# Kernel tuning notes

Hardware: AMD Instinct MI355X
Metric: run time of the kernel (lower is better)

## Reference

```python
import jax, jax.numpy as jnp
import numpy as np

COST_CLASS, COST_MASK, COST_DICE = 2.0, 5.0, 5.0
NUM_POINTS = 12544

def setup_inputs() -> dict:
    key = jax.random.key(0)
    k1, k2, k3, k4, k5 = jax.random.split(key, 5)
    bs, Q, K = 4, 100, 134
    H = W = 256
    M = 80
    P = H * W
    pred_logits = jax.random.normal(k1, (bs, Q, K), dtype=jnp.float32)
    pred_masks = jax.random.normal(k2, (bs, Q, H, W), dtype=jnp.float32)
    tgt_labels = jax.random.randint(k3, (M,), 0, K - 1, dtype=jnp.int32)
    # binary target masks, stored as float (matches .float() in torch code)
    tgt_masks = (jax.random.uniform(k4, (M, H, W)) > 0.5).astype(jnp.float32)
    # random subset of points without replacement (torch.randperm[:num_points])
    point_idx = jax.random.permutation(k5, P)[:NUM_POINTS].astype(jnp.int32)
    return {"pred_logits": pred_logits, "pred_masks": pred_masks,
            "tgt_labels": tgt_labels, "tgt_masks": tgt_masks,
            "point_idx": point_idx}

def reference(pred_logits, pred_masks, tgt_labels, tgt_masks, point_idx):
    bs, Q, K = pred_logits.shape
    N = bs * Q
    M = tgt_masks.shape[0]
    Pn = point_idx.shape[0]

    # class cost: -p[n, tgt_id[m]]
    out_prob = jax.nn.softmax(pred_logits.reshape(N, K), axis=-1)
    tgt_ids = jnp.clip(tgt_labels.astype(jnp.int32), 0, K - 1)
    cost_class = -out_prob[:, tgt_ids]                      # (N, M)

    # sampled mask logits / targets
    x = pred_masks.reshape(N, -1)[:, point_idx]             # (N, Pn) logits
    y = tgt_masks.reshape(M, -1)[:, point_idx]              # (M, Pn) binary float

    # BCE-with-logits cost, separable form:
    # mean_p[softplus(x) - x*y] = mean_p softplus(x) - (x @ y^T)/Pn
    sp_mean = jnp.mean(jax.nn.softplus(x), axis=-1)         # (N,)
    xy = jnp.einsum('np,mp->nm', x, y)                      # (N, M)
    cost_mask = sp_mean[:, None] - xy / Pn

    # dice cost
    s = jax.nn.sigmoid(x)                                   # (N, Pn)
    numer = 2.0 * jnp.einsum('np,mp->nm', s, y)             # (N, M)
    denom = jnp.sum(s, axis=-1)[:, None] + jnp.sum(y, axis=-1)[None, :]
    cost_dice = 1.0 - (numer + 1.0) / (denom + 1.0)

    C = COST_CLASS * cost_class + COST_MASK * cost_mask + COST_DICE * cost_dice
    return C.reshape(bs, Q, M)
```

## Files before the change

### kernel.cpp

```cpp
#include <hip/hip_runtime.h>
#include <math.h>

#define N_ROWS 400
#define M_ROWS 80
#define K_CLS  134
#define PN     12544
#define PFULL  65536
#define NSUB   25
#define TSTEPS 392
#define KSPLIT 196
#define TPB    2
#define KCG    49

#define GY_BLOCKS 245

typedef __attribute__((ext_vector_type(4))) float  f32x4;
typedef __attribute__((ext_vector_type(8))) __bf16 bf16x8;

__device__ __forceinline__ float wave_reduce_sum(float v) {
#pragma unroll
    for (int off = 32; off > 0; off >>= 1) v += __shfl_down(v, off, 64);
    return v;
}

__global__ __launch_bounds__(1024) void sort_softmax_kernel(
        const int* __restrict__ point_idx, int* __restrict__ sel,
        const float* __restrict__ pred_logits,
        float* __restrict__ rowmax, float* __restrict__ rowsum) {
    int tid = threadIdx.x;
    if (blockIdx.x == 0) {
        __shared__ unsigned int bits[PFULL / 32];
        __shared__ int wtot[16], wbase[16];
        bits[tid] = 0u; bits[tid + 1024] = 0u;
        __syncthreads();
        for (int i = tid; i < PN; i += 1024) {
            int p = point_idx[i];
            atomicOr(&bits[p >> 5], 1u << (p & 31));
        }
        __syncthreads();
        unsigned int w0 = bits[tid * 2], w1 = bits[tid * 2 + 1];
        int cnt = __popc(w0) + __popc(w1);
        int lane = tid & 63, wid = tid >> 6;
        int v = cnt;
#pragma unroll
        for (int off = 1; off < 64; off <<= 1) {
            int u = __shfl_up(v, off, 64);
            if (lane >= off) v += u;
        }
        if (lane == 63) wtot[wid] = v;
        __syncthreads();
        if (tid == 0) {
            int run = 0;
#pragma unroll
            for (int i = 0; i < 16; ++i) { wbase[i] = run; run += wtot[i]; }
        }
        __syncthreads();
        int base = wbase[wid] + (v - cnt);
        int p0 = tid * 64;
        while (w0) { int b = __builtin_ctz(w0); w0 &= w0 - 1; sel[base++] = p0 + b; }
        p0 += 32;
        while (w1) { int b = __builtin_ctz(w1); w1 &= w1 - 1; sel[base++] = p0 + b; }
    } else {
        int wave = tid >> 6, lane = tid & 63;
        int n = (blockIdx.x - 1) * 16 + wave;
        const float* row = pred_logits + n * K_CLS;
        float mx = -1e30f;
        for (int k = lane; k < K_CLS; k += 64) mx = fmaxf(mx, row[k]);
#pragma unroll
        for (int off = 32; off > 0; off >>= 1) mx = fmaxf(mx, __shfl_down(mx, off, 64));
        mx = __shfl(mx, 0, 64);
        float se = 0.f;
        for (int k = lane; k < K_CLS; k += 64) se += expf(row[k] - mx);
        se = wave_reduce_sum(se);
        if (lane == 0) { rowmax[n] = mx; rowsum[n] = se; }
    }
}

__global__ __launch_bounds__(512) void gather_y_kernel(
        const float* __restrict__ tgt_masks, const int* __restrict__ sel,
        __bf16* __restrict__ Yb, float* __restrict__ ypart) {
    __shared__ float smem[128];
    int b = blockIdx.x;
    int j = b / 49, tch = b % 49;
    int wave = threadIdx.x >> 6, lane = threadIdx.x & 63;
    int colL = lane & 15, quad = lane >> 4;
    int m = 16 * j + colL;
    int t = tch * 8 + wave;
    int k0 = t * 32 + quad * 8;
    const float* yrow = tgt_masks + (size_t)m * PFULL;
    int idx[8];
    *(int4*)(idx)     = *(const int4*)(sel + k0);
    *(int4*)(idx + 4) = *(const int4*)(sel + k0 + 4);
    bf16x8 v; float acc = 0.f;
#pragma unroll
    for (int jj = 0; jj < 8; ++jj) {
        float y = yrow[idx[jj]];
        v[jj] = (__bf16)y;
        acc += y;
    }
    ((bf16x8*)Yb)[(size_t)(t * 5 + j) * 64 + lane] = v;
    acc += __shfl_down(acc, 32, 64);
    acc += __shfl_down(acc, 16, 64);
    if (quad == 0) smem[wave * 16 + colL] = acc;
    __syncthreads();
    if (threadIdx.x < 16) {
        float s = 0.f;
#pragma unroll
        for (int wv = 0; wv < 8; ++wv) s += smem[wv * 16 + threadIdx.x];
        ypart[tch * M_ROWS + 16 * j + threadIdx.x] = s;
    }
}

__global__ __launch_bounds__(256) void gemm_fused_kernel(
        const float* __restrict__ pred_masks, const int* __restrict__ sel,
        const __bf16* __restrict__ Yb,
        float* __restrict__ xypart, float* __restrict__ sypart,
        float* __restrict__ rowS, float* __restrict__ rowSP) {
    __shared__ float red[4][40][64];
    __shared__ float rowred[4][2][16];
    int wave = threadIdx.x >> 6, lane = threadIdx.x & 63;
    int nsub = blockIdx.x / KCG, kcg = blockIdx.x % KCG;
    int kc = kcg * 4 + wave;
    int n0 = nsub * 16;
    int colL = lane & 15, quad = lane >> 4;
    int tbase = kc * TPB;

    const float* row = pred_masks + (size_t)(n0 + colL) * PFULL;
    const bf16x8* Yfrag = (const bf16x8*)Yb;

    f32x4 accX[5], accS[5];
    f32x4 zero = {0.f, 0.f, 0.f, 0.f};
#pragma unroll
    for (int j = 0; j < 5; ++j) { accX[j] = zero; accS[j] = zero; }
    float sumS = 0.f, sumSP = 0.f;

    float xs[TPB][8];
    bf16x8 Bbuf[TPB][5];
#pragma unroll
    for (int i = 0; i < TPB; ++i) {
        int t = tbase + i;
        int k0 = t * 32 + quad * 8;
        int idx[8];
        *(int4*)(idx)     = *(const int4*)(sel + k0);
        *(int4*)(idx + 4) = *(const int4*)(sel + k0 + 4);
#pragma unroll
        for (int jj = 0; jj < 8; ++jj) xs[i][jj] = row[idx[jj]];
        const bf16x8* q = Yfrag + (size_t)(t * 5) * 64 + lane;
#pragma unroll
        for (int j = 0; j < 5; ++j) Bbuf[i][j] = q[(size_t)j * 64];
    }
#pragma unroll
    for (int i = 0; i < TPB; ++i) {
        bf16x8 aX, aS;
#pragma unroll
        for (int jj = 0; jj < 8; ++jj) {
            float x  = xs[i][jj];
            float ax = fabsf(x);
            float e  = __expf(-ax);
            float inv = __builtin_amdgcn_rcpf(1.f + e);
            float sig = (x >= 0.f) ? inv : e * inv;
            float sp  = fmaxf(x, 0.f) + __logf(1.f + e);
            aX[jj] = (__bf16)x; aS[jj] = (__bf16)sig;
            sumS += sig; sumSP += sp;
        }
#pragma unroll
        for (int j = 0; j < 5; ++j) {
            accX[j] = __builtin_amdgcn_mfma_f32_16x16x32_bf16(aX, Bbuf[i][j], accX[j], 0, 0, 0);
            accS[j] = __builtin_amdgcn_mfma_f32_16x16x32_bf16(aS, Bbuf[i][j], accS[j], 0, 0, 0);
        }
    }

#pragma unroll
    for (int j = 0; j < 5; ++j)
#pragma unroll
        for (int r = 0; r < 4; ++r) {
            red[wave][j * 4 + r][lane]      = accX[j][r];
            red[wave][20 + j * 4 + r][lane] = accS[j][r];
        }
    sumS  += __shfl_down(sumS, 32, 64);
    sumS  += __shfl_down(sumS, 16, 64);
    sumSP += __shfl_down(sumSP, 32, 64);
    sumSP += __shfl_down(sumSP, 16, 64);
    if (lane < 16) { rowred[wave][0][lane] = sumS; rowred[wave][1][lane] = sumSP; }
    __syncthreads();
#pragma unroll
    for (int v0 = 0; v0 < 10; ++v0) {
        int v = wave * 10 + v0;
        float s = red[0][v][lane] + red[1][v][lane] + red[2][v][lane] + red[3][v][lane];
        int vv = (v < 20) ? v : v - 20;
        int j = vv >> 2, r = vv & 3;
        int n = n0 + quad * 4 + r, m = 16 * j + colL;
        float* dst = (v < 20) ? xypart : sypart;
        dst[(size_t)kcg * (N_ROWS * M_ROWS) + n * M_ROWS + m] = s;
    }
    if (threadIdx.x < 16) {
        rowS[kcg * N_ROWS + n0 + threadIdx.x] =
            rowred[0][0][threadIdx.x] + rowred[1][0][threadIdx.x] +
            rowred[2][0][threadIdx.x] + rowred[3][0][threadIdx.x];
    } else if (threadIdx.x < 32) {
        int l = threadIdx.x - 16;
        rowSP[kcg * N_ROWS + n0 + l] =
            rowred[0][1][l] + rowred[1][1][l] + rowred[2][1][l] + rowred[3][1][l];
    }
}

__global__ void combine_kernel(const float* __restrict__ logits,
                               const int* __restrict__ tgt_labels,
                               const float* __restrict__ rowmax,
                               const float* __restrict__ rowsum,
                               const float* __restrict__ rowS,
                               const float* __restrict__ rowSP,
                               const float* __restrict__ ypart,
                               const float* __restrict__ xypart,
                               const float* __restrict__ sypart,
                               float* __restrict__ out) {
    int idx = blockIdx.x * blockDim.x + threadIdx.x;
    if (idx >= N_ROWS * M_ROWS) return;
    int n = idx / M_ROWS, m = idx % M_ROWS;
    float xy = 0.f, sy = 0.f, ssumv = 0.f, spsumv = 0.f, ysum = 0.f;
#pragma unroll 7
    for (int g = 0; g < KCG; ++g) {
        xy += xypart[(size_t)g * (N_ROWS * M_ROWS) + idx];
        sy += sypart[(size_t)g * (N_ROWS * M_ROWS) + idx];
        ssumv  += rowS[g * N_ROWS + n];
        spsumv += rowSP[g * N_ROWS + n];
        ysum += ypart[g * M_ROWS + m];
    }
    int tid = tgt_labels[m];
    tid = min(max(tid, 0), K_CLS - 1);
    float p = expf(logits[n * K_CLS + tid] - rowmax[n]) / rowsum[n];
    float cost_class = -p;
    float cost_mask = (spsumv - xy) * (1.0f / PN);
    float cost_dice = 1.f - (2.f * sy + 1.f) / (ssumv + ysum + 1.f);
    out[idx] = 2.f * cost_class + 5.f * cost_mask + 5.f * cost_dice;
}

extern "C" void kernel_launch(void* const* d_in, const int* in_sizes, int n_in,
                              void* d_out, int out_size, void* d_ws, size_t ws_size,
                              hipStream_t stream) {
    const float* pred_logits = (const float*)d_in[0];
    const float* pred_masks  = (const float*)d_in[1];
    const int*   tgt_labels  = (const int*)d_in[2];
    const float* tgt_masks   = (const float*)d_in[3];
    const int*   point_idx   = (const int*)d_in[4];
    float* out = (float*)d_out;

    char* ws = (char*)d_ws;
    size_t off = 0;
    auto carve = [&](size_t nbytes) {
        char* p = ws + off;
        off += (nbytes + 255) & ~(size_t)255;
        return p;
    };
    int*   sel    = (int*)carve(PN * 4);
    float* rowmax = (float*)carve(N_ROWS * 4);
    float* rowsum = (float*)carve(N_ROWS * 4);
    float* ypart  = (float*)carve(KCG * M_ROWS * 4);
    float* rowS   = (float*)carve(KCG * N_ROWS * 4);
    float* rowSP  = (float*)carve(KCG * N_ROWS * 4);
    float* xypart = (float*)carve((size_t)KCG * N_ROWS * M_ROWS * 4);
    float* sypart = (float*)carve((size_t)KCG * N_ROWS * M_ROWS * 4);
    __bf16* Yb = (__bf16*)carve((size_t)TSTEPS * 5 * 1024);
    (void)ws_size; (void)in_sizes; (void)n_in; (void)out_size;

    sort_softmax_kernel<<<26, 1024, 0, stream>>>(point_idx, sel, pred_logits, rowmax, rowsum);
    gather_y_kernel<<<GY_BLOCKS, 512, 0, stream>>>(tgt_masks, sel, Yb, ypart);
    gemm_fused_kernel<<<NSUB * KCG, 256, 0, stream>>>(
        pred_masks, sel, Yb, xypart, sypart, rowS, rowSP);
    combine_kernel<<<(N_ROWS * M_ROWS + 255) / 256, 256, 0, stream>>>(
        pred_logits, tgt_labels, rowmax, rowsum, rowS, rowSP, ypart, xypart, sypart, out);
}
```

Before: 219.3 us.

## Stream-compact sampled mask points into dense buffers before GEMM

```diff
diff --git a/kernel.cpp b/kernel.cpp
--- a/kernel.cpp
+++ b/kernel.cpp
@@ -6,14 +6,18 @@
 #define K_CLS  134
 #define PN     12544
 #define PFULL  65536
+#define WORDS  (PFULL / 32)
 #define NSUB   25
 #define TSTEPS 392
-#define KSPLIT 196
 #define TPB    2
 #define KCG    49
 
 #define GY_BLOCKS 245
 
+#define CROWS  (N_ROWS + M_ROWS)
+#define CHUNK  16384
+#define CPB    (PFULL / CHUNK)
+
 typedef __attribute__((ext_vector_type(4))) float  f32x4;
 typedef __attribute__((ext_vector_type(8))) __bf16 bf16x8;
 
@@ -24,12 +28,13 @@
 }
 
 __global__ __launch_bounds__(1024) void sort_softmax_kernel(
-        const int* __restrict__ point_idx, int* __restrict__ sel,
+        const int* __restrict__ point_idx,
+        unsigned int* __restrict__ bitmap_g, int* __restrict__ rank_g,
         const float* __restrict__ pred_logits,
         float* __restrict__ rowmax, float* __restrict__ rowsum) {
     int tid = threadIdx.x;
     if (blockIdx.x == 0) {
-        __shared__ unsigned int bits[PFULL / 32];
+        __shared__ unsigned int bits[WORDS];
         __shared__ int wtot[16], wbase[16];
         bits[tid] = 0u; bits[tid + 1024] = 0u;
         __syncthreads();
@@ -56,10 +61,10 @@
         }
         __syncthreads();
         int base = wbase[wid] + (v - cnt);
-        int p0 = tid * 64;
-        while (w0) { int b = __builtin_ctz(w0); w0 &= w0 - 1; sel[base++] = p0 + b; }
-        p0 += 32;
-        while (w1) { int b = __builtin_ctz(w1); w1 &= w1 - 1; sel[base++] = p0 + b; }
+        bitmap_g[tid * 2]     = w0;
+        bitmap_g[tid * 2 + 1] = w1;
+        rank_g[tid * 2]       = base;
+        rank_g[tid * 2 + 1]   = base + __popc(w0);
     } else {
         int wave = tid >> 6, lane = tid & 63;
         int n = (blockIdx.x - 1) * 16 + wave;
@@ -76,8 +81,47 @@
     }
 }
 
+__global__ __launch_bounds__(256) void compact_kernel(
+        const float* __restrict__ pred_masks, const float* __restrict__ tgt_masks,
+        const unsigned int* __restrict__ bitmap_g, const int* __restrict__ rank_g,
+        float* __restrict__ Xc, float* __restrict__ Yc) {
+    __shared__ unsigned int sb[CHUNK / 32];
+    __shared__ int swb[CHUNK / 32];
+    int b   = blockIdx.x;
+    int row = b / CPB, ch = b % CPB;
+    int tid = threadIdx.x;
+    int w0  = ch * (CHUNK / 32);
+    sb[tid]        = bitmap_g[w0 + tid];
+    sb[tid + 256]  = bitmap_g[w0 + tid + 256];
+    swb[tid]       = rank_g[w0 + tid];
+    swb[tid + 256] = rank_g[w0 + tid + 256];
+    __syncthreads();
+
+    const float* src; float* dst;
+    if (row < N_ROWS) {
+        src = pred_masks + (size_t)row * PFULL;
+        dst = Xc + (size_t)row * PN;
+    } else {
+        src = tgt_masks + (size_t)(row - N_ROWS) * PFULL;
+        dst = Yc + (size_t)(row - N_ROWS) * PN;
+    }
+    int p0 = ch * CHUNK;
+#pragma unroll
+    for (int it = 0; it < CHUNK / (256 * 4); ++it) {
+        int e = (it * 256 + tid) * 4;
+        f32x4 v = *(const f32x4*)(src + p0 + e);
+        unsigned int w = sb[e >> 5];
+        int r = swb[e >> 5] + __popc(w & ((1u << (e & 31)) - 1u));
+        unsigned int m4 = (w >> (e & 31)) & 0xFu;
+        if (m4 & 1u) { dst[r++] = v[0]; }
+        if (m4 & 2u) { dst[r++] = v[1]; }
+        if (m4 & 4u) { dst[r++] = v[2]; }
+        if (m4 & 8u) { dst[r]   = v[3]; }
+    }
+}
+
 __global__ __launch_bounds__(512) void gather_y_kernel(
-        const float* __restrict__ tgt_masks, const int* __restrict__ sel,
+        const float* __restrict__ Yc,
         __bf16* __restrict__ Yb, float* __restrict__ ypart) {
     __shared__ float smem[128];
     int b = blockIdx.x;
@@ -87,16 +131,14 @@
     int m = 16 * j + colL;
     int t = tch * 8 + wave;
     int k0 = t * 32 + quad * 8;
-    const float* yrow = tgt_masks + (size_t)m * PFULL;
-    int idx[8];
-    *(int4*)(idx)     = *(const int4*)(sel + k0);
-    *(int4*)(idx + 4) = *(const int4*)(sel + k0 + 4);
+    const float* yrow = Yc + (size_t)m * PN;
+    f32x4 a = *(const f32x4*)(yrow + k0);
+    f32x4 c = *(const f32x4*)(yrow + k0 + 4);
     bf16x8 v; float acc = 0.f;
 #pragma unroll
-    for (int jj = 0; jj < 8; ++jj) {
-        float y = yrow[idx[jj]];
-        v[jj] = (__bf16)y;
-        acc += y;
+    for (int jj = 0; jj < 4; ++jj) {
+        v[jj]     = (__bf16)a[jj]; acc += a[jj];
+        v[jj + 4] = (__bf16)c[jj]; acc += c[jj];
     }
     ((bf16x8*)Yb)[(size_t)(t * 5 + j) * 64 + lane] = v;
     acc += __shfl_down(acc, 32, 64);
@@ -112,7 +154,7 @@
 }
 
 __global__ __launch_bounds__(256) void gemm_fused_kernel(
-        const float* __restrict__ pred_masks, const int* __restrict__ sel,
+        const float* __restrict__ Xc,
         const __bf16* __restrict__ Yb,
         float* __restrict__ xypart, float* __restrict__ sypart,
         float* __restrict__ rowS, float* __restrict__ rowSP) {
@@ -125,7 +167,7 @@
     int colL = lane & 15, quad = lane >> 4;
     int tbase = kc * TPB;
 
-    const float* row = pred_masks + (size_t)(n0 + colL) * PFULL;
+    const float* row = Xc + (size_t)(n0 + colL) * PN;
     const bf16x8* Yfrag = (const bf16x8*)Yb;
 
     f32x4 accX[5], accS[5];
@@ -140,11 +182,10 @@
     for (int i = 0; i < TPB; ++i) {
         int t = tbase + i;
         int k0 = t * 32 + quad * 8;
-        int idx[8];
-        *(int4*)(idx)     = *(const int4*)(sel + k0);
-        *(int4*)(idx + 4) = *(const int4*)(sel + k0 + 4);
-#pragma unroll
-        for (int jj = 0; jj < 8; ++jj) xs[i][jj] = row[idx[jj]];
+        f32x4 a = *(const f32x4*)(row + k0);
+        f32x4 c = *(const f32x4*)(row + k0 + 4);
+#pragma unroll
+        for (int jj = 0; jj < 4; ++jj) { xs[i][jj] = a[jj]; xs[i][jj + 4] = c[jj]; }
         const bf16x8* q = Yfrag + (size_t)(t * 5) * 64 + lane;
 #pragma unroll
         for (int j = 0; j < 5; ++j) Bbuf[i][j] = q[(size_t)j * 64];
@@ -252,7 +293,8 @@
         off += (nbytes + 255) & ~(size_t)255;
         return p;
     };
-    int*   sel    = (int*)carve(PN * 4);
+    unsigned int* bitmap = (unsigned int*)carve(WORDS * 4);
+    int*   rankp  = (int*)carve(WORDS * 4);
     float* rowmax = (float*)carve(N_ROWS * 4);
     float* rowsum = (float*)carve(N_ROWS * 4);
     float* ypart  = (float*)carve(KCG * M_ROWS * 4);
@@ -261,12 +303,17 @@
     float* xypart = (float*)carve((size_t)KCG * N_ROWS * M_ROWS * 4);
     float* sypart = (float*)carve((size_t)KCG * N_ROWS * M_ROWS * 4);
     __bf16* Yb = (__bf16*)carve((size_t)TSTEPS * 5 * 1024);
+    float* Xc = (float*)carve((size_t)N_ROWS * PN * 4);
+    float* Yc = (float*)carve((size_t)M_ROWS * PN * 4);
     (void)ws_size; (void)in_sizes; (void)n_in; (void)out_size;
 
-    sort_softmax_kernel<<<26, 1024, 0, stream>>>(point_idx, sel, pred_logits, rowmax, rowsum);
-    gather_y_kernel<<<GY_BLOCKS, 512, 0, stream>>>(tgt_masks, sel, Yb, ypart);
+    sort_softmax_kernel<<<26, 1024, 0, stream>>>(point_idx, bitmap, rankp,
+                                                 pred_logits, rowmax, rowsum);
+    compact_kernel<<<CROWS * CPB, 256, 0, stream>>>(pred_masks, tgt_masks,
+                                                    bitmap, rankp, Xc, Yc);
+    gather_y_kernel<<<GY_BLOCKS, 512, 0, stream>>>(Yc, Yb, ypart);
     gemm_fused_kernel<<<NSUB * KCG, 256, 0, stream>>>(
-        pred_masks, sel, Yb, xypart, sypart, rowS, rowSP);
+        Xc, Yb, xypart, sypart, rowS, rowSP);
     combine_kernel<<<(N_ROWS * M_ROWS + 255) / 256, 256, 0, stream>>>(
         pred_logits, tgt_labels, rowmax, rowsum, rowS, rowSP, ypart, xypart, sypart, out);
 }
```

After: 223.0 us. No clear change (+1.7%).

## Replace index gather with dense streaming over all points using selection bitmaps

Applied to the files above, without the earlier changes.

```diff
diff --git a/kernel.cpp b/kernel.cpp
--- a/kernel.cpp
+++ b/kernel.cpp
@@ -6,13 +6,11 @@
 #define K_CLS  134
 #define PN     12544
 #define PFULL  65536
+#define WORDS  (PFULL / 32)
 #define NSUB   25
-#define TSTEPS 392
-#define KSPLIT 196
-#define TPB    2
-#define KCG    49
-
-#define GY_BLOCKS 245
+#define KS     32
+#define TCH    (WORDS / KS)
+#define NM     (N_ROWS * M_ROWS)
 
 typedef __attribute__((ext_vector_type(4))) float  f32x4;
 typedef __attribute__((ext_vector_type(8))) __bf16 bf16x8;
@@ -24,13 +22,13 @@
 }
 
 __global__ __launch_bounds__(1024) void sort_softmax_kernel(
-        const int* __restrict__ point_idx, int* __restrict__ sel,
+        const int* __restrict__ point_idx,
+        unsigned int* __restrict__ bitmap_g,
         const float* __restrict__ pred_logits,
         float* __restrict__ rowmax, float* __restrict__ rowsum) {
     int tid = threadIdx.x;
     if (blockIdx.x == 0) {
-        __shared__ unsigned int bits[PFULL / 32];
-        __shared__ int wtot[16], wbase[16];
+        __shared__ unsigned int bits[WORDS];
         bits[tid] = 0u; bits[tid + 1024] = 0u;
         __syncthreads();
         for (int i = tid; i < PN; i += 1024) {
@@ -38,28 +36,8 @@
             atomicOr(&bits[p >> 5], 1u << (p & 31));
         }
         __syncthreads();
-        unsigned int w0 = bits[tid * 2], w1 = bits[tid * 2 + 1];
-        int cnt = __popc(w0) + __popc(w1);
-        int lane = tid & 63, wid = tid >> 6;
-        int v = cnt;
-#pragma unroll
-        for (int off = 1; off < 64; off <<= 1) {
-            int u = __shfl_up(v, off, 64);
-            if (lane >= off) v += u;
-        }
-        if (lane == 63) wtot[wid] = v;
-        __syncthreads();
-        if (tid == 0) {
-            int run = 0;
-#pragma unroll
-            for (int i = 0; i < 16; ++i) { wbase[i] = run; run += wtot[i]; }
-        }
-        __syncthreads();
-        int base = wbase[wid] + (v - cnt);
-        int p0 = tid * 64;
-        while (w0) { int b = __builtin_ctz(w0); w0 &= w0 - 1; sel[base++] = p0 + b; }
-        p0 += 32;
-        while (w1) { int b = __builtin_ctz(w1); w1 &= w1 - 1; sel[base++] = p0 + b; }
+        bitmap_g[tid]        = bits[tid];
+        bitmap_g[tid + 1024] = bits[tid + 1024];
     } else {
         int wave = tid >> 6, lane = tid & 63;
         int n = (blockIdx.x - 1) * 16 + wave;
@@ -76,57 +54,65 @@
     }
 }
 
-__global__ __launch_bounds__(512) void gather_y_kernel(
-        const float* __restrict__ tgt_masks, const int* __restrict__ sel,
-        __bf16* __restrict__ Yb, float* __restrict__ ypart) {
-    __shared__ float smem[128];
+__global__ __launch_bounds__(256) void buildY_kernel(
+        const float* __restrict__ tgt_masks,
+        const unsigned int* __restrict__ bitmap_g,
+        unsigned int* __restrict__ yb_g, float* __restrict__ ypart) {
+    __shared__ float smem[4];
     int b = blockIdx.x;
-    int j = b / 49, tch = b % 49;
+    int m = b >> 3, ch = b & 7;
     int wave = threadIdx.x >> 6, lane = threadIdx.x & 63;
-    int colL = lane & 15, quad = lane >> 4;
-    int m = 16 * j + colL;
-    int t = tch * 8 + wave;
-    int k0 = t * 32 + quad * 8;
-    const float* yrow = tgt_masks + (size_t)m * PFULL;
-    int idx[8];
-    *(int4*)(idx)     = *(const int4*)(sel + k0);
-    *(int4*)(idx + 4) = *(const int4*)(sel + k0 + 4);
-    bf16x8 v; float acc = 0.f;
-#pragma unroll
-    for (int jj = 0; jj < 8; ++jj) {
-        float y = yrow[idx[jj]];
-        v[jj] = (__bf16)y;
-        acc += y;
-    }
-    ((bf16x8*)Yb)[(size_t)(t * 5 + j) * 64 + lane] = v;
-    acc += __shfl_down(acc, 32, 64);
-    acc += __shfl_down(acc, 16, 64);
-    if (quad == 0) smem[wave * 16 + colL] = acc;
-    __syncthreads();
-    if (threadIdx.x < 16) {
-        float s = 0.f;
-#pragma unroll
-        for (int wv = 0; wv < 8; ++wv) s += smem[wv * 16 + threadIdx.x];
-        ypart[tch * M_ROWS + 16 * j + threadIdx.x] = s;
-    }
-}
-
-__global__ __launch_bounds__(256) void gemm_fused_kernel(
-        const float* __restrict__ pred_masks, const int* __restrict__ sel,
-        const __bf16* __restrict__ Yb,
+    const float* row = tgt_masks + (size_t)m * PFULL + ch * 8192 + wave * 2048;
+    unsigned int* dst = yb_g + (size_t)m * WORDS + ch * 256 + wave * 64;
+    const unsigned int* selw = bitmap_g + ch * 256 + wave * 64;
+    int cnt = 0;
+    for (int it = 0; it < 32; ++it) {
+        float v = row[it * 64 + lane];
+        unsigned long long bal = __ballot(v > 0.5f);
+        unsigned int lo = (unsigned int)bal & selw[it * 2];
+        unsigned int hi = (unsigned int)(bal >> 32) & selw[it * 2 + 1];
+        if (lane == 0) { dst[it * 2] = lo; cnt += __popc(lo) + __popc(hi); }
+        if (lane == 1) dst[it * 2 + 1] = hi;
+    }
+    if (lane == 0) smem[wave] = (float)cnt;
+    __syncthreads();
+    if (threadIdx.x == 0)
+        ypart[ch * M_ROWS + m] = smem[0] + smem[1] + smem[2] + smem[3];
+}
+
+__global__ __launch_bounds__(256) void gemm_full_kernel(
+        const float* __restrict__ pred_masks,
+        const unsigned int* __restrict__ bitmap_g,
+        const unsigned int* __restrict__ yb_g,
         float* __restrict__ xypart, float* __restrict__ sypart,
         float* __restrict__ rowS, float* __restrict__ rowSP) {
     __shared__ float red[4][40][64];
     __shared__ float rowred[4][2][16];
-    int wave = threadIdx.x >> 6, lane = threadIdx.x & 63;
-    int nsub = blockIdx.x / KCG, kcg = blockIdx.x % KCG;
-    int kc = kcg * 4 + wave;
+    __shared__ __align__(8) unsigned int lut[32];
+    unsigned int* ybl  = (unsigned int*)red;
+    unsigned int* sell = ((unsigned int*)red) + TCH * 80;
+
+    int tid = threadIdx.x;
+    int wave = tid >> 6, lane = tid & 63;
+    int colL = lane & 15, quad = lane >> 4;
+    int nsub = blockIdx.x / KS, ch = blockIdx.x % KS;
     int n0 = nsub * 16;
-    int colL = lane & 15, quad = lane >> 4;
-    int tbase = kc * TPB;
-
-    const float* row = pred_masks + (size_t)(n0 + colL) * PFULL;
-    const bf16x8* Yfrag = (const bf16x8*)Yb;
+    int t0 = ch * TCH;
+
+    if (tid < 16) {
+        unsigned int lo = ((tid & 1) ? 0x3F80u : 0u) | ((tid & 2) ? 0x3F800000u : 0u);
+        unsigned int hi = ((tid & 4) ? 0x3F80u : 0u) | ((tid & 8) ? 0x3F800000u : 0u);
+        lut[tid * 2] = lo; lut[tid * 2 + 1] = hi;
+    }
+    for (int i = tid; i < M_ROWS * TCH; i += 256) {
+        int m = i >> 6, tl = i & 63;
+        ybl[tl * 80 + m] = yb_g[(size_t)m * WORDS + t0 + tl];
+    }
+    for (int i = tid; i < TCH; i += 256) sell[i] = bitmap_g[t0 + i];
+    __syncthreads();
+
+    const float* rowp = pred_masks + (size_t)(n0 + colL) * PFULL;
+    const uint2* lutp = (const uint2*)lut;
 
     f32x4 accX[5], accS[5];
     f32x4 zero = {0.f, 0.f, 0.f, 0.f};
@@ -134,42 +120,48 @@
     for (int j = 0; j < 5; ++j) { accX[j] = zero; accS[j] = zero; }
     float sumS = 0.f, sumSP = 0.f;
 
-    float xs[TPB][8];
-    bf16x8 Bbuf[TPB][5];
-#pragma unroll
-    for (int i = 0; i < TPB; ++i) {
-        int t = tbase + i;
-        int k0 = t * 32 + quad * 8;
-        int idx[8];
-        *(int4*)(idx)     = *(const int4*)(sel + k0);
-        *(int4*)(idx + 4) = *(const int4*)(sel + k0 + 4);
-#pragma unroll
-        for (int jj = 0; jj < 8; ++jj) xs[i][jj] = row[idx[jj]];
-        const bf16x8* q = Yfrag + (size_t)(t * 5) * 64 + lane;
-#pragma unroll
-        for (int j = 0; j < 5; ++j) Bbuf[i][j] = q[(size_t)j * 64];
-    }
-#pragma unroll
-    for (int i = 0; i < TPB; ++i) {
+    int tl0 = wave * 16;
+    int kbase = (t0 + tl0) * 32 + quad * 8;
+    f32x4 pa = *(const f32x4*)(rowp + kbase);
+    f32x4 pb = *(const f32x4*)(rowp + kbase + 4);
+
+#pragma unroll 4
+    for (int i = 0; i < 16; ++i) {
+        int tl = tl0 + i;
+        f32x4 xa = pa, xb = pb;
+        if (i < 15) {
+            int kn = kbase + (i + 1) * 32;
+            pa = *(const f32x4*)(rowp + kn);
+            pb = *(const f32x4*)(rowp + kn + 4);
+        }
+        unsigned int mb = (sell[tl] >> (quad * 8)) & 0xFFu;
+        float xsv[8];
+        *(f32x4*)(xsv) = xa; *(f32x4*)(xsv + 4) = xb;
         bf16x8 aX, aS;
 #pragma unroll
         for (int jj = 0; jj < 8; ++jj) {
-            float x  = xs[i][jj];
+            float x  = xsv[jj];
             float ax = fabsf(x);
             float e  = __expf(-ax);
             float inv = __builtin_amdgcn_rcpf(1.f + e);
             float sig = (x >= 0.f) ? inv : e * inv;
             float sp  = fmaxf(x, 0.f) + __logf(1.f + e);
             aX[jj] = (__bf16)x; aS[jj] = (__bf16)sig;
-            sumS += sig; sumSP += sp;
+            if (mb & (1u << jj)) { sumS += sig; sumSP += sp; }
         }
 #pragma unroll
         for (int j = 0; j < 5; ++j) {
-            accX[j] = __builtin_amdgcn_mfma_f32_16x16x32_bf16(aX, Bbuf[i][j], accX[j], 0, 0, 0);
-            accS[j] = __builtin_amdgcn_mfma_f32_16x16x32_bf16(aS, Bbuf[i][j], accS[j], 0, 0, 0);
-        }
-    }
-
+            unsigned int w  = ybl[tl * 80 + 16 * j + colL];
+            unsigned int by = (w >> (quad * 8)) & 0xFFu;
+            union { bf16x8 v; uint2 u[2]; } Bb;
+            Bb.u[0] = lutp[by & 15u];
+            Bb.u[1] = lutp[by >> 4];
+            accX[j] = __builtin_amdgcn_mfma_f32_16x16x32_bf16(aX, Bb.v, accX[j], 0, 0, 0);
+            accS[j] = __builtin_amdgcn_mfma_f32_16x16x32_bf16(aS, Bb.v, accS[j], 0, 0, 0);
+        }
+    }
+
+    __syncthreads();
 #pragma unroll
     for (int j = 0; j < 5; ++j)
 #pragma unroll
@@ -191,16 +183,17 @@
         int j = vv >> 2, r = vv & 3;
         int n = n0 + quad * 4 + r, m = 16 * j + colL;
         float* dst = (v < 20) ? xypart : sypart;
-        dst[(size_t)kcg * (N_ROWS * M_ROWS) + n * M_ROWS + m] = s;
-    }
-    if (threadIdx.x < 16) {
-        rowS[kcg * N_ROWS + n0 + threadIdx.x] =
-            rowred[0][0][threadIdx.x] + rowred[1][0][threadIdx.x] +
-            rowred[2][0][threadIdx.x] + rowred[3][0][threadIdx.x];
-    } else if (threadIdx.x < 32) {
-        int l = threadIdx.x - 16;
-        rowSP[kcg * N_ROWS + n0 + l] =
-            rowred[0][1][l] + rowred[1][1][l] + rowred[2][1][l] + rowred[3][1][l];
+        dst[(size_t)ch * NM + n * M_ROWS + m] = s;
+    }
+    if (tid < 16) {
+        rowS[ch * N_ROWS + n0 + tid] =
+            rowred[0][0][tid] + rowred[1][0][tid] +
+            rowred[2][0][tid] + rowred[3][0][tid];
+    } else if (tid < 32) {
+        int l = tid - 16;
+        rowSP[ch * N_ROWS + n0 + l] =
+            rowred[0][1][l] + rowred[1][1][l] +
+            rowred[2][1][l] + rowred[3][1][l];
     }
 }
 
@@ -215,17 +208,18 @@
                                const float* __restrict__ sypart,
                                float* __restrict__ out) {
     int idx = blockIdx.x * blockDim.x + threadIdx.x;
-    if (idx >= N_ROWS * M_ROWS) return;
+    if (idx >= NM) return;
     int n = idx / M_ROWS, m = idx % M_ROWS;
     float xy = 0.f, sy = 0.f, ssumv = 0.f, spsumv = 0.f, ysum = 0.f;
-#pragma unroll 7
-    for (int g = 0; g < KCG; ++g) {
-        xy += xypart[(size_t)g * (N_ROWS * M_ROWS) + idx];
-        sy += sypart[(size_t)g * (N_ROWS * M_ROWS) + idx];
+#pragma unroll 8
+    for (int g = 0; g < KS; ++g) {
+        xy += xypart[(size_t)g * NM + idx];
+        sy += sypart[(size_t)g * NM + idx];
         ssumv  += rowS[g * N_ROWS + n];
         spsumv += rowSP[g * N_ROWS + n];
-        ysum += ypart[g * M_ROWS + m];
-    }
+    }
+#pragma unroll
+    for (int g = 0; g < 8; ++g) ysum += ypart[g * M_ROWS + m];
     int tid = tgt_labels[m];
     tid = min(max(tid, 0), K_CLS - 1);
     float p = expf(logits[n * K_CLS + tid] - rowmax[n]) / rowsum[n];
@@ -252,21 +246,23 @@
         off += (nbytes + 255) & ~(size_t)255;
         return p;
     };
-    int*   sel    = (int*)carve(PN * 4);
+    unsigned int* bitmap = (unsigned int*)carve(WORDS * 4);
+    unsigned int* yb     = (unsigned int*)carve((size_t)M_ROWS * WORDS * 4);
     float* rowmax = (float*)carve(N_ROWS * 4);
     float* rowsum = (float*)carve(N_ROWS * 4);
-    float* ypart  = (float*)carve(KCG * M_ROWS * 4);
-    float* rowS   = (float*)carve(KCG * N_ROWS * 4);
-    float* rowSP  = (float*)carve(KCG * N_ROWS * 4);
-    float* xypart = (float*)carve((size_t)KCG * N_ROWS * M_ROWS * 4);
-    float* sypart = (float*)carve((size_t)KCG * N_ROWS * M_ROWS * 4);
-    __bf16* Yb = (__bf16*)carve((size_t)TSTEPS * 5 * 1024);
+    float* ypart  = (float*)carve(8 * M_ROWS * 4);
+    float* rowS   = (float*)carve(KS * N_ROWS * 4);
+    float* rowSP  = (float*)carve(KS * N_ROWS * 4);
+    float* xypart = (float*)carve((size_t)KS * NM * 4);
+    float* sypart = (float*)carve((size_t)KS * NM * 4);
     (void)ws_size; (void)in_sizes; (void)n_in; (void)out_size;
 
-    sort_softmax_kernel<<<26, 1024, 0, stream>>>(point_idx, sel, pred_logits, rowmax, rowsum);
-    gather_y_kernel<<<GY_BLOCKS, 512, 0, stream>>>(tgt_masks, sel, Yb, ypart);
-    gemm_fused_kernel<<<NSUB * KCG, 256, 0, stream>>>(
-        pred_masks, sel, Yb, xypart, sypart, rowS, rowSP);
-    combine_kernel<<<(N_ROWS * M_ROWS + 255) / 256, 256, 0, stream>>>(
-        pred_logits, tgt_labels, rowmax, rowsum, rowS, rowSP, ypart, xypart, sypart, out);
-}
+    sort_softmax_kernel<<<26, 1024, 0, stream>>>(point_idx, bitmap,
+                                                 pred_logits, rowmax, rowsum);
+    buildY_kernel<<<M_ROWS * 8, 256, 0, stream>>>(tgt_masks, bitmap, yb, ypart);
+    gemm_full_kernel<<<NSUB * KS, 256, 0, stream>>>(
+        pred_masks, bitmap, yb, xypart, sypart, rowS, rowSP);
+    combine_kernel<<<(NM + 255) / 256, 256, 0, stream>>>(
+        pred_logits, tgt_labels, rowmax, rowsum, rowS, rowSP, ypart,
+        xypart, sypart, out);
+}
```

Result: slower. 230.1 us (+4.9%).
